# Performance work log

Measured on AMD Instinct MI355X. Metric: run time of the kernel, lower is better.

The kernel has to match this reference:

```python
import jax, jax.numpy as jnp
import numpy as np

N = 50000
E = 600000
D = 128
OUT = 40
NUM_ITERS = 5
GAMMA = 0.1
EPS = 0.1


def setup_inputs() -> dict:
    key = jax.random.key(0)
    ks = jax.random.split(key, 10)
    x = jax.random.normal(ks[0], (N, D), dtype=jnp.float32)
    edge_index = jax.random.randint(ks[1], (2, E), 0, N, dtype=jnp.int64)
    edge_weight = jax.random.uniform(ks[2], (E,), dtype=jnp.float32)
    s = 1.0 / np.sqrt(D)
    W_emb = jax.random.uniform(ks[3], (D, D), jnp.float32, -s, s)
    b_emb = jax.random.uniform(ks[4], (D,), jnp.float32, -s, s)
    W_lin = jax.random.uniform(ks[5], (D, D), jnp.float32, -s, s)
    W_anti = jax.random.uniform(ks[6], (D, D), jnp.float32, -s, s)
    b_conv = jax.random.uniform(ks[7], (D,), jnp.float32, -s, s)
    W_out = jax.random.uniform(ks[8], (OUT, D), jnp.float32, -s, s)
    b_out = jax.random.uniform(ks[9], (OUT,), jnp.float32, -s, s)
    return {"x": x, "edge_index": edge_index, "edge_weight": edge_weight,
            "W_emb": W_emb, "b_emb": b_emb, "W_lin": W_lin, "W_anti": W_anti,
            "b_conv": b_conv, "W_out": W_out, "b_out": b_out}


def reference(x, edge_index, edge_weight, W_emb, b_emb, W_lin, W_anti, b_conv, W_out, b_out):
    # input embedding: Linear(input_dim, hidden_dim)
    x = x @ W_emb.T + b_emb

    src = edge_index[0]  # x_j (messages gathered from source)
    dst = edge_index[1]  # aggregated at target via scatter-add

    # antisymmetric weight: W - W^T - gamma*I
    A = W_anti - W_anti.T - GAMMA * jnp.eye(D, dtype=x.dtype)

    def step(x, _):
        neigh = x @ W_lin.T                      # [N, D] linear transform
        msgs = neigh[src] * edge_weight[:, None]  # [E, D] gather + weight
        agg = jax.ops.segment_sum(msgs, dst, num_segments=N)  # scatter-add
        conv = x @ A.T + agg + b_conv
        x = x + EPS * jnp.tanh(conv)
        return x, None

    x, _ = jax.lax.scan(step, x, None, length=NUM_ITERS)

    # readout
    return x @ W_out.T + b_out
```

## Files before the change

kernel.cpp:

```cpp
#include <hip/hip_runtime.h>
#include <math.h>

#define N_NODES 50000
#define E_EDGES 600000
#define D_DIM 128
#define OUT_DIM 40
#define N_ITERS 5
#define GAMMA_C 0.1f
#define EPS_C 0.1f
#define SCAN_BLOCKS 196
#define GEMM_BLOCKS 391
#define CONV_BLOCKS 782
#define EDGE_BLOCKS_C 293

typedef short v8s __attribute__((ext_vector_type(8)));
typedef float v4f __attribute__((ext_vector_type(4)));
typedef unsigned int uint;
typedef unsigned short ushort;

__device__ __forceinline__ ushort f2bf(float f) {
    union { float f; uint u; } v; v.f = f;
    uint u = v.u;
    uint r = 0x7fffu + ((u >> 16) & 1u);
    return (ushort)((u + r) >> 16);
}
__device__ __forceinline__ float bf2f(ushort h) {
    union { uint u; float f; } v; v.u = ((uint)h) << 16;
    return v.f;
}
__device__ __forceinline__ float bflo(uint u) {
    union { uint u; float f; } v; v.u = u << 16; return v.f;
}
__device__ __forceinline__ float bfhi(uint u) {
    union { uint u; float f; } v; v.u = u & 0xffff0000u; return v.f;
}

__device__ __forceinline__ float tanh_fast(float x) {
    float e = __expf(x + x);
    return 1.0f - 2.0f * __builtin_amdgcn_rcpf(e + 1.0f);
}

__global__ __launch_bounds__(256) void zero_prep_kernel(int* __restrict__ cursor,
                                                        const float* __restrict__ Wemb,
                                                        const float* __restrict__ Wlin,
                                                        const float* __restrict__ Wanti,
                                                        const float* __restrict__ Wout,
                                                        ushort* __restrict__ WembH,
                                                        ushort* __restrict__ Wcat2H,
                                                        ushort* __restrict__ WoutH) {
    int i = blockIdx.x * 256 + threadIdx.x;
    if (i < N_NODES) cursor[i] = 0;
    if (i < D_DIM * D_DIM) {
        int r = i >> 7, c = i & 127;
        WembH[i] = f2bf(Wemb[i]);
        float a = Wanti[r * 128 + c] - Wanti[c * 128 + r];
        if (r == c) a -= GAMMA_C;
        Wcat2H[r * 256 + c]       = f2bf(a);
        Wcat2H[r * 256 + 128 + c] = f2bf(Wlin[r * 128 + c]);
        if (i < 48 * 128) WoutH[i] = (r < OUT_DIM) ? f2bf(Wout[r * 128 + c]) : (ushort)0;
    }
}

__global__ __launch_bounds__(256) void build_embed_kernel(
        const float* __restrict__ Xf, const ushort* __restrict__ Wh,
        const float* __restrict__ bias, ushort* __restrict__ xH,
        const int* __restrict__ src, const int* __restrict__ dst,
        const float* __restrict__ ew, int* __restrict__ cursor,
        int2* __restrict__ es2, int M) {
    __shared__ ushort Xs[128 * 128];
    const int tid = threadIdx.x;

    if (blockIdx.x >= GEMM_BLOCKS) {
        int base = (blockIdx.x - GEMM_BLOCKS) * 2048 + tid;
#pragma unroll
        for (int k = 0; k < 8; ++k) {
            int e = base + k * 256;
            if (e < E_EDGES) {
                int d = dst[e];
                int pos = atomicAdd(&cursor[d], 1);
                es2[pos] = make_int2(src[e], __float_as_int(ew[e]));
            }
        }
        return;
    }

    const int rowBase = blockIdx.x * 128;
#pragma unroll
    for (int p = 0; p < 8; ++p) {
        int cid = p * 256 + tid;
        int r = cid >> 4, c8 = cid & 15;
        int gr = rowBase + r;
        uint4 val = make_uint4(0, 0, 0, 0);
        if (gr < M) {
            const float* ptr = Xf + (size_t)gr * 128 + c8 * 8;
            float4 f0 = *(const float4*)ptr;
            float4 f1 = *(const float4*)(ptr + 4);
            val.x = (uint)f2bf(f0.x) | ((uint)f2bf(f0.y) << 16);
            val.y = (uint)f2bf(f0.z) | ((uint)f2bf(f0.w) << 16);
            val.z = (uint)f2bf(f1.x) | ((uint)f2bf(f1.y) << 16);
            val.w = (uint)f2bf(f1.z) | ((uint)f2bf(f1.w) << 16);
        }
        *(uint4*)(Xs + r * 128 + ((c8 ^ (r & 7)) << 3)) = val;
    }
    __syncthreads();

    const int lane = tid & 63;
    const int wv = tid >> 6;
    const int wrow = (wv & 1) * 64;
    const int wcol = (wv >> 1) * 64;
    const int l16 = lane & 15;
    const int q = lane >> 4;

    v4f acc[4][4];
#pragma unroll
    for (int i = 0; i < 4; ++i)
#pragma unroll
        for (int j = 0; j < 4; ++j) { v4f z = {0.f,0.f,0.f,0.f}; acc[i][j] = z; }

#pragma unroll
    for (int ks = 0; ks < 4; ++ks) {
        const int chunk = ks * 4 + q;
        v8s a[4], b[4];
#pragma unroll
        for (int i = 0; i < 4; ++i) {
            int m = wrow + i * 16 + l16;
            a[i] = *(const v8s*)(Xs + m * 128 + ((chunk ^ (m & 7)) << 3));
        }
#pragma unroll
        for (int j = 0; j < 4; ++j)
            b[j] = *(const v8s*)(Wh + (size_t)(wcol + j * 16 + l16) * 128 + chunk * 8);
#pragma unroll
        for (int i = 0; i < 4; ++i)
#pragma unroll
            for (int j = 0; j < 4; ++j)
                acc[i][j] = __builtin_amdgcn_mfma_f32_16x16x32_bf16(a[i], b[j], acc[i][j], 0, 0, 0);
    }

#pragma unroll
    for (int j = 0; j < 4; ++j) {
        int col = wcol + j * 16 + l16;
        float bj = bias[col];
#pragma unroll
        for (int i = 0; i < 4; ++i) {
            int grB = rowBase + wrow + i * 16 + q * 4;
#pragma unroll
            for (int r = 0; r < 4; ++r) {
                int gr = grB + r;
                if (gr < M) xH[(size_t)gr * 128 + col] = f2bf(acc[i][j][r] + bj);
            }
        }
    }
}

__global__ __launch_bounds__(512) void gather_conv_update(
        const ushort* __restrict__ xin, ushort* __restrict__ xout,
        const int2* __restrict__ es2, const int* __restrict__ rowStart,
        const int* __restrict__ rowEnd, const ushort* __restrict__ Wcat2,
        const float* __restrict__ bconv, const ushort* __restrict__ WoutH,
        const float* __restrict__ bout, float* __restrict__ out,
        int doOut, int M) {
    __shared__ ushort Xs0[64 * 128];
    __shared__ ushort Xs1[64 * 128];
    const int tid = threadIdx.x;
    const int rowBase = blockIdx.x * 64;

#pragma unroll
    for (int p = 0; p < 2; ++p) {
        int cid = p * 512 + tid;
        int r = cid >> 4, c8 = cid & 15;
        int gr = rowBase + r;
        uint4 xv = make_uint4(0, 0, 0, 0);
        if (gr < M) xv = *(const uint4*)(xin + (size_t)gr * 128 + c8 * 8);
        *(uint4*)(Xs1 + r * 128 + ((c8 ^ (r & 7)) << 3)) = xv;
    }

    const int q16 = tid & 15;
    const int nb = tid >> 4;
    const int gb = tid & 48;
    for (int pass = 0; pass < 2; ++pass) {
        int r = pass * 32 + nb;
        int gr = rowBase + r;
        float sA[8] = {0,0,0,0,0,0,0,0};
        float sB[8] = {0,0,0,0,0,0,0,0};
        int e0 = 0, deg = 0;
        if (gr < M) { e0 = rowStart[gr]; deg = rowEnd[gr] - e0; }
        for (int base = 0; base < deg; base += 16) {
            int idx = e0 + base + q16;
            int2 myE = es2[idx < E_EDGES ? idx : E_EDGES - 1];
            int cnt = deg - base; if (cnt > 16) cnt = 16;
            int k = 0;
            for (; k + 4 <= cnt; k += 4) {
                int s0 = __shfl(myE.x, gb + k + 0);
                int s1 = __shfl(myE.x, gb + k + 1);
                int s2 = __shfl(myE.x, gb + k + 2);
                int s3 = __shfl(myE.x, gb + k + 3);
                float w0 = __int_as_float(__shfl(myE.y, gb + k + 0));
                float w1 = __int_as_float(__shfl(myE.y, gb + k + 1));
                float w2 = __int_as_float(__shfl(myE.y, gb + k + 2));
                float w3 = __int_as_float(__shfl(myE.y, gb + k + 3));
                uint4 v0 = *(const uint4*)(xin + (size_t)s0 * 128 + q16 * 8);
                uint4 v1 = *(const uint4*)(xin + (size_t)s1 * 128 + q16 * 8);
                uint4 v2 = *(const uint4*)(xin + (size_t)s2 * 128 + q16 * 8);
                uint4 v3 = *(const uint4*)(xin + (size_t)s3 * 128 + q16 * 8);
                sA[0] = fmaf(w0, bflo(v0.x), sA[0]); sA[1] = fmaf(w0, bfhi(v0.x), sA[1]);
                sA[2] = fmaf(w0, bflo(v0.y), sA[2]); sA[3] = fmaf(w0, bfhi(v0.y), sA[3]);
                sA[4] = fmaf(w0, bflo(v0.z), sA[4]); sA[5] = fmaf(w0, bfhi(v0.z), sA[5]);
                sA[6] = fmaf(w0, bflo(v0.w), sA[6]); sA[7] = fmaf(w0, bfhi(v0.w), sA[7]);
                sB[0] = fmaf(w1, bflo(v1.x), sB[0]); sB[1] = fmaf(w1, bfhi(v1.x), sB[1]);
                sB[2] = fmaf(w1, bflo(v1.y), sB[2]); sB[3] = fmaf(w1, bfhi(v1.y), sB[3]);
                sB[4] = fmaf(w1, bflo(v1.z), sB[4]); sB[5] = fmaf(w1, bfhi(v1.z), sB[5]);
                sB[6] = fmaf(w1, bflo(v1.w), sB[6]); sB[7] = fmaf(w1, bfhi(v1.w), sB[7]);
                sA[0] = fmaf(w2, bflo(v2.x), sA[0]); sA[1] = fmaf(w2, bfhi(v2.x), sA[1]);
                sA[2] = fmaf(w2, bflo(v2.y), sA[2]); sA[3] = fmaf(w2, bfhi(v2.y), sA[3]);
                sA[4] = fmaf(w2, bflo(v2.z), sA[4]); sA[5] = fmaf(w2, bfhi(v2.z), sA[5]);
                sA[6] = fmaf(w2, bflo(v2.w), sA[6]); sA[7] = fmaf(w2, bfhi(v2.w), sA[7]);
                sB[0] = fmaf(w3, bflo(v3.x), sB[0]); sB[1] = fmaf(w3, bfhi(v3.x), sB[1]);
                sB[2] = fmaf(w3, bflo(v3.y), sB[2]); sB[3] = fmaf(w3, bfhi(v3.y), sB[3]);
                sB[4] = fmaf(w3, bflo(v3.z), sB[4]); sB[5] = fmaf(w3, bfhi(v3.z), sB[5]);
                sB[6] = fmaf(w3, bflo(v3.w), sB[6]); sB[7] = fmaf(w3, bfhi(v3.w), sB[7]);
            }
            for (; k < cnt; ++k) {
                int s = __shfl(myE.x, gb + k);
                float w = __int_as_float(__shfl(myE.y, gb + k));
                uint4 v = *(const uint4*)(xin + (size_t)s * 128 + q16 * 8);
                sA[0] = fmaf(w, bflo(v.x), sA[0]); sA[1] = fmaf(w, bfhi(v.x), sA[1]);
                sA[2] = fmaf(w, bflo(v.y), sA[2]); sA[3] = fmaf(w, bfhi(v.y), sA[3]);
                sA[4] = fmaf(w, bflo(v.z), sA[4]); sA[5] = fmaf(w, bfhi(v.z), sA[5]);
                sA[6] = fmaf(w, bflo(v.w), sA[6]); sA[7] = fmaf(w, bfhi(v.w), sA[7]);
            }
        }
        uint4 o;
        o.x = (uint)f2bf(sA[0] + sB[0]) | ((uint)f2bf(sA[1] + sB[1]) << 16);
        o.y = (uint)f2bf(sA[2] + sB[2]) | ((uint)f2bf(sA[3] + sB[3]) << 16);
        o.z = (uint)f2bf(sA[4] + sB[4]) | ((uint)f2bf(sA[5] + sB[5]) << 16);
        o.w = (uint)f2bf(sA[6] + sB[6]) | ((uint)f2bf(sA[7] + sB[7]) << 16);
        *(uint4*)(Xs0 + r * 128 + ((q16 ^ (r & 7)) << 3)) = o;
    }
    __syncthreads();

    const int lane = tid & 63;
    const int wv = tid >> 6;
    const int l16 = lane & 15;
    const int q = lane >> 4;

    v4f acc[4];
#pragma unroll
    for (int i = 0; i < 4; ++i) { v4f z = {0.f,0.f,0.f,0.f}; acc[i] = z; }

#pragma unroll
    for (int ks = 0; ks < 8; ++ks) {
        const ushort* Xsrc = (ks < 4) ? Xs0 : Xs1;
        const int wOff = (ks < 4) ? 128 : 0;
        const int chunk = (ks & 3) * 4 + q;
        v8s a[4], b;
#pragma unroll
        for (int i = 0; i < 4; ++i) {
            int m = i * 16 + l16;
            a[i] = *(const v8s*)(Xsrc + m * 128 + ((chunk ^ (m & 7)) << 3));
        }
        b = *(const v8s*)(Wcat2 + (size_t)(wv * 16 + l16) * 256 + wOff + chunk * 8);
#pragma unroll
        for (int i = 0; i < 4; ++i)
            acc[i] = __builtin_amdgcn_mfma_f32_16x16x32_bf16(a[i], b, acc[i], 0, 0, 0);
    }

    if (doOut) __syncthreads();

    {
        int col = wv * 16 + l16;
        float bj = bconv[col];
        const int csw = col >> 3, clo = col & 7;
#pragma unroll
        for (int i = 0; i < 4; ++i) {
            int trB = i * 16 + q * 4;
#pragma unroll
            for (int r = 0; r < 4; ++r) {
                int tr = trB + r;
                int gr = rowBase + tr;
                if (gr < M) {
                    int li = tr * 128 + (((csw ^ (tr & 7)) << 3) | clo);
                    float conv = acc[i][r] + bj;
                    float xv = bf2f(Xs1[li]) + EPS_C * tanh_fast(conv);
                    ushort h = f2bf(xv);
                    xout[(size_t)gr * 128 + col] = h;
                    if (doOut) Xs1[li] = h;
                }
            }
        }
    }

    if (doOut) {
        __syncthreads();
        if (wv < 4) {
            v4f acc2[3];
#pragma unroll
            for (int j = 0; j < 3; ++j) { v4f z = {0.f,0.f,0.f,0.f}; acc2[j] = z; }

#pragma unroll
            for (int ks = 0; ks < 4; ++ks) {
                const int chunk = ks * 4 + q;
                int m = wv * 16 + l16;
                v8s a2 = *(const v8s*)(Xs1 + m * 128 + ((chunk ^ (m & 7)) << 3));
                v8s b2[3];
#pragma unroll
                for (int j = 0; j < 3; ++j)
                    b2[j] = *(const v8s*)(WoutH + (size_t)(j * 16 + l16) * 128 + chunk * 8);
#pragma unroll
                for (int j = 0; j < 3; ++j)
                    acc2[j] = __builtin_amdgcn_mfma_f32_16x16x32_bf16(a2, b2[j], acc2[j], 0, 0, 0);
            }

#pragma unroll
            for (int j = 0; j < 3; ++j) {
                int col = j * 16 + l16;
                if (col >= OUT_DIM) continue;
                float bj = bout[col];
                int grB = rowBase + wv * 16 + q * 4;
#pragma unroll
                for (int r = 0; r < 4; ++r) {
                    int gr = grB + r;
                    if (gr < M) out[(size_t)gr * OUT_DIM + col] = acc2[j][r] + bj;
                }
            }
        }
    }
}

__global__ __launch_bounds__(256) void hist_kernel(const int* __restrict__ dst,
                                                   int* __restrict__ cnt) {
    int base = blockIdx.x * 2048 + threadIdx.x;
#pragma unroll
    for (int k = 0; k < 8; ++k) {
        int e = base + k * 256;
        if (e < E_EDGES) atomicAdd(&cnt[dst[e]], 1);
    }
}

__global__ __launch_bounds__(256) void scan_phase1(const int* __restrict__ deg,
                                                   int* __restrict__ localEx,
                                                   int* __restrict__ blockSums) {
    __shared__ int tmp[256];
    const int t = threadIdx.x;
    const int i = blockIdx.x * 256 + t;
    int v = (i < N_NODES) ? deg[i] : 0;
    tmp[t] = v;
    __syncthreads();
#pragma unroll
    for (int off = 1; off < 256; off <<= 1) {
        int u = (t >= off) ? tmp[t - off] : 0;
        __syncthreads();
        tmp[t] += u;
        __syncthreads();
    }
    if (i < N_NODES) localEx[i] = tmp[t] - v;
    if (t == 255) blockSums[blockIdx.x] = tmp[255];
}

__global__ __launch_bounds__(256) void scan_phase23(int* __restrict__ rowStart,
                                                    const int* __restrict__ blockSums,
                                                    int* __restrict__ cursor) {
    __shared__ int tmp[256];
    __shared__ int offs;
    const int t = threadIdx.x;
    int v = (t < SCAN_BLOCKS) ? blockSums[t] : 0;
    tmp[t] = v;
    __syncthreads();
#pragma unroll
    for (int off = 1; off < 256; off <<= 1) {
        int u = (t >= off) ? tmp[t - off] : 0;
        __syncthreads();
        tmp[t] += u;
        __syncthreads();
    }
    if (t == blockIdx.x) offs = tmp[t] - v;
    __syncthreads();
    const int i = blockIdx.x * 256 + t;
    if (i < N_NODES) {
        int val = rowStart[i] + offs;
        rowStart[i] = val;
        cursor[i] = val;
    }
}

extern "C" void kernel_launch(void* const* d_in, const int* in_sizes, int n_in,
                              void* d_out, int out_size, void* d_ws, size_t ws_size,
                              hipStream_t stream) {
    const float* x_in   = (const float*)d_in[0];
    const int*   ei     = (const int*)  d_in[1];
    const float* ew     = (const float*)d_in[2];
    const float* W_emb  = (const float*)d_in[3];
    const float* b_emb  = (const float*)d_in[4];
    const float* W_lin  = (const float*)d_in[5];
    const float* W_anti = (const float*)d_in[6];
    const float* b_conv = (const float*)d_in[7];
    const float* W_out  = (const float*)d_in[8];
    const float* b_out  = (const float*)d_in[9];
    float* out = (float*)d_out;

    ushort* xhA    = (ushort*)d_ws;
    ushort* xhB    = xhA + (size_t)N_NODES * D_DIM;
    ushort* WembH  = xhB + (size_t)N_NODES * D_DIM;
    ushort* Wcat2H = WembH + D_DIM * D_DIM;
    ushort* WoutH  = Wcat2H + 2 * D_DIM * D_DIM;
    int*    rowStart = (int*)(WoutH + 48 * D_DIM);
    int*    cursor   = rowStart + N_NODES;
    int2*   es2      = (int2*)(cursor + N_NODES);
    int*    blockSums = (int*)(es2 + E_EDGES);

    const int* src = ei;
    const int* dst = ei + E_EDGES;

    zero_prep_kernel<<<SCAN_BLOCKS, 256, 0, stream>>>(cursor, W_emb, W_lin, W_anti,
                                                      W_out, WembH, Wcat2H, WoutH);
    hist_kernel<<<EDGE_BLOCKS_C, 256, 0, stream>>>(dst, cursor);
    scan_phase1<<<SCAN_BLOCKS, 256, 0, stream>>>(cursor, rowStart, blockSums);
    scan_phase23<<<SCAN_BLOCKS, 256, 0, stream>>>(rowStart, blockSums, cursor);
    build_embed_kernel<<<GEMM_BLOCKS + EDGE_BLOCKS_C, 256, 0, stream>>>(
        x_in, WembH, b_emb, xhA, src, dst, ew, cursor, es2, N_NODES);

    ushort* bufs[2] = { xhA, xhB };
    for (int it = 0; it < N_ITERS; ++it) {
        gather_conv_update<<<CONV_BLOCKS, 512, 0, stream>>>(
            bufs[it & 1], bufs[(it + 1) & 1], es2, rowStart, cursor,
            Wcat2H, b_conv, WoutH, b_out, out,
            (it == N_ITERS - 1) ? 1 : 0, N_NODES);
    }
}
```

Baseline: 378.5 us.

## Halve rows per conv block, raise occupancy, unroll edge gather by eight

The fused gather/conv/update kernel now handles 32 rows per block instead of 64. That halves its shared memory and doubles the block count, and a min-blocks launch bound requests higher occupancy. The edge-gather loop gains an 8-wide unrolled path so more independent row loads are in flight, and the readout GEMM is redistributed over 6 waves. The aim is to hide the latency of the irregular gathers. In exchange, each block reuses the weight tile for fewer rows and may face register pressure under the occupancy bound.

```diff
diff --git a/kernel.cpp b/kernel.cpp
--- a/kernel.cpp
+++ b/kernel.cpp
@@ -10,7 +10,7 @@
 #define EPS_C 0.1f
 #define SCAN_BLOCKS 196
 #define GEMM_BLOCKS 391
-#define CONV_BLOCKS 782
+#define CONV_BLOCKS 1563
 #define EDGE_BLOCKS_C 293
 
 typedef short v8s __attribute__((ext_vector_type(8)));
@@ -152,22 +152,20 @@
     }
 }
 
-__global__ __launch_bounds__(512) void gather_conv_update(
+__global__ __launch_bounds__(512, 8) void gather_conv_update(
         const ushort* __restrict__ xin, ushort* __restrict__ xout,
         const int2* __restrict__ es2, const int* __restrict__ rowStart,
         const int* __restrict__ rowEnd, const ushort* __restrict__ Wcat2,
         const float* __restrict__ bconv, const ushort* __restrict__ WoutH,
         const float* __restrict__ bout, float* __restrict__ out,
         int doOut, int M) {
-    __shared__ ushort Xs0[64 * 128];
-    __shared__ ushort Xs1[64 * 128];
+    __shared__ ushort Xs0[32 * 128];
+    __shared__ ushort Xs1[32 * 128];
     const int tid = threadIdx.x;
-    const int rowBase = blockIdx.x * 64;
-
-#pragma unroll
-    for (int p = 0; p < 2; ++p) {
-        int cid = p * 512 + tid;
-        int r = cid >> 4, c8 = cid & 15;
+    const int rowBase = blockIdx.x * 32;
+
+    {
+        int r = tid >> 4, c8 = tid & 15;
         int gr = rowBase + r;
         uint4 xv = make_uint4(0, 0, 0, 0);
         if (gr < M) xv = *(const uint4*)(xin + (size_t)gr * 128 + c8 * 8);
@@ -177,8 +175,8 @@
     const int q16 = tid & 15;
     const int nb = tid >> 4;
     const int gb = tid & 48;
-    for (int pass = 0; pass < 2; ++pass) {
-        int r = pass * 32 + nb;
+    {
+        int r = nb;
         int gr = rowBase + r;
         float sA[8] = {0,0,0,0,0,0,0,0};
         float sB[8] = {0,0,0,0,0,0,0,0};
@@ -189,6 +187,64 @@
             int2 myE = es2[idx < E_EDGES ? idx : E_EDGES - 1];
             int cnt = deg - base; if (cnt > 16) cnt = 16;
             int k = 0;
+            for (; k + 8 <= cnt; k += 8) {
+                int s0 = __shfl(myE.x, gb + k + 0);
+                int s1 = __shfl(myE.x, gb + k + 1);
+                int s2 = __shfl(myE.x, gb + k + 2);
+                int s3 = __shfl(myE.x, gb + k + 3);
+                int s4 = __shfl(myE.x, gb + k + 4);
+                int s5 = __shfl(myE.x, gb + k + 5);
+                int s6 = __shfl(myE.x, gb + k + 6);
+                int s7 = __shfl(myE.x, gb + k + 7);
+                float w0 = __int_as_float(__shfl(myE.y, gb + k + 0));
+                float w1 = __int_as_float(__shfl(myE.y, gb + k + 1));
+                float w2 = __int_as_float(__shfl(myE.y, gb + k + 2));
+                float w3 = __int_as_float(__shfl(myE.y, gb + k + 3));
+                float w4 = __int_as_float(__shfl(myE.y, gb + k + 4));
+                float w5 = __int_as_float(__shfl(myE.y, gb + k + 5));
+                float w6 = __int_as_float(__shfl(myE.y, gb + k + 6));
+                float w7 = __int_as_float(__shfl(myE.y, gb + k + 7));
+                uint4 v0 = *(const uint4*)(xin + (size_t)s0 * 128 + q16 * 8);
+                uint4 v1 = *(const uint4*)(xin + (size_t)s1 * 128 + q16 * 8);
+                uint4 v2 = *(const uint4*)(xin + (size_t)s2 * 128 + q16 * 8);
+                uint4 v3 = *(const uint4*)(xin + (size_t)s3 * 128 + q16 * 8);
+                uint4 v4 = *(const uint4*)(xin + (size_t)s4 * 128 + q16 * 8);
+                uint4 v5 = *(const uint4*)(xin + (size_t)s5 * 128 + q16 * 8);
+                uint4 v6 = *(const uint4*)(xin + (size_t)s6 * 128 + q16 * 8);
+                uint4 v7 = *(const uint4*)(xin + (size_t)s7 * 128 + q16 * 8);
+                sA[0] = fmaf(w0, bflo(v0.x), sA[0]); sA[1] = fmaf(w0, bfhi(v0.x), sA[1]);
+                sA[2] = fmaf(w0, bflo(v0.y), sA[2]); sA[3] = fmaf(w0, bfhi(v0.y), sA[3]);
+                sA[4] = fmaf(w0, bflo(v0.z), sA[4]); sA[5] = fmaf(w0, bfhi(v0.z), sA[5]);
+                sA[6] = fmaf(w0, bflo(v0.w), sA[6]); sA[7] = fmaf(w0, bfhi(v0.w), sA[7]);
+                sB[0] = fmaf(w1, bflo(v1.x), sB[0]); sB[1] = fmaf(w1, bfhi(v1.x), sB[1]);
+                sB[2] = fmaf(w1, bflo(v1.y), sB[2]); sB[3] = fmaf(w1, bfhi(v1.y), sB[3]);
+                sB[4] = fmaf(w1, bflo(v1.z), sB[4]); sB[5] = fmaf(w1, bfhi(v1.z), sB[5]);
+                sB[6] = fmaf(w1, bflo(v1.w), sB[6]); sB[7] = fmaf(w1, bfhi(v1.w), sB[7]);
+                sA[0] = fmaf(w2, bflo(v2.x), sA[0]); sA[1] = fmaf(w2, bfhi(v2.x), sA[1]);
+                sA[2] = fmaf(w2, bflo(v2.y), sA[2]); sA[3] = fmaf(w2, bfhi(v2.y), sA[3]);
+                sA[4] = fmaf(w2, bflo(v2.z), sA[4]); sA[5] = fmaf(w2, bfhi(v2.z), sA[5]);
+                sA[6] = fmaf(w2, bflo(v2.w), sA[6]); sA[7] = fmaf(w2, bfhi(v2.w), sA[7]);
+                sB[0] = fmaf(w3, bflo(v3.x), sB[0]); sB[1] = fmaf(w3, bfhi(v3.x), sB[1]);
+                sB[2] = fmaf(w3, bflo(v3.y), sB[2]); sB[3] = fmaf(w3, bfhi(v3.y), sB[3]);
+                sB[4] = fmaf(w3, bflo(v3.z), sB[4]); sB[5] = fmaf(w3, bfhi(v3.z), sB[5]);
+                sB[6] = fmaf(w3, bflo(v3.w), sB[6]); sB[7] = fmaf(w3, bfhi(v3.w), sB[7]);
+                sA[0] = fmaf(w4, bflo(v4.x), sA[0]); sA[1] = fmaf(w4, bfhi(v4.x), sA[1]);
+                sA[2] = fmaf(w4, bflo(v4.y), sA[2]); sA[3] = fmaf(w4, bfhi(v4.y), sA[3]);
+                sA[4] = fmaf(w4, bflo(v4.z), sA[4]); sA[5] = fmaf(w4, bfhi(v4.z), sA[5]);
+                sA[6] = fmaf(w4, bflo(v4.w), sA[6]); sA[7] = fmaf(w4, bfhi(v4.w), sA[7]);
+                sB[0] = fmaf(w5, bflo(v5.x), sB[0]); sB[1] = fmaf(w5, bfhi(v5.x), sB[1]);
+                sB[2] = fmaf(w5, bflo(v5.y), sB[2]); sB[3] = fmaf(w5, bfhi(v5.y), sB[3]);
+                sB[4] = fmaf(w5, bflo(v5.z), sB[4]); sB[5] = fmaf(w5, bfhi(v5.z), sB[5]);
+                sB[6] = fmaf(w5, bflo(v5.w), sB[6]); sB[7] = fmaf(w5, bfhi(v5.w), sB[7]);
+                sA[0] = fmaf(w6, bflo(v6.x), sA[0]); sA[1] = fmaf(w6, bfhi(v6.x), sA[1]);
+                sA[2] = fmaf(w6, bflo(v6.y), sA[2]); sA[3] = fmaf(w6, bfhi(v6.y), sA[3]);
+                sA[4] = fmaf(w6, bflo(v6.z), sA[4]); sA[5] = fmaf(w6, bfhi(v6.z), sA[5]);
+                sA[6] = fmaf(w6, bflo(v6.w), sA[6]); sA[7] = fmaf(w6, bfhi(v6.w), sA[7]);
+                sB[0] = fmaf(w7, bflo(v7.x), sB[0]); sB[1] = fmaf(w7, bfhi(v7.x), sB[1]);
+                sB[2] = fmaf(w7, bflo(v7.y), sB[2]); sB[3] = fmaf(w7, bfhi(v7.y), sB[3]);
+                sB[4] = fmaf(w7, bflo(v7.z), sB[4]); sB[5] = fmaf(w7, bfhi(v7.z), sB[5]);
+                sB[6] = fmaf(w7, bflo(v7.w), sB[6]); sB[7] = fmaf(w7, bfhi(v7.w), sB[7]);
+            }
             for (; k + 4 <= cnt; k += 4) {
                 int s0 = __shfl(myE.x, gb + k + 0);
                 int s1 = __shfl(myE.x, gb + k + 1);
@@ -243,24 +299,24 @@
     const int l16 = lane & 15;
     const int q = lane >> 4;
 
-    v4f acc[4];
-#pragma unroll
-    for (int i = 0; i < 4; ++i) { v4f z = {0.f,0.f,0.f,0.f}; acc[i] = z; }
+    v4f acc[2];
+#pragma unroll
+    for (int i = 0; i < 2; ++i) { v4f z = {0.f,0.f,0.f,0.f}; acc[i] = z; }
 
 #pragma unroll
     for (int ks = 0; ks < 8; ++ks) {
         const ushort* Xsrc = (ks < 4) ? Xs0 : Xs1;
         const int wOff = (ks < 4) ? 128 : 0;
         const int chunk = (ks & 3) * 4 + q;
-        v8s a[4], b;
-#pragma unroll
-        for (int i = 0; i < 4; ++i) {
+        v8s a[2], b;
+#pragma unroll
+        for (int i = 0; i < 2; ++i) {
             int m = i * 16 + l16;
             a[i] = *(const v8s*)(Xsrc + m * 128 + ((chunk ^ (m & 7)) << 3));
         }
         b = *(const v8s*)(Wcat2 + (size_t)(wv * 16 + l16) * 256 + wOff + chunk * 8);
 #pragma unroll
-        for (int i = 0; i < 4; ++i)
+        for (int i = 0; i < 2; ++i)
             acc[i] = __builtin_amdgcn_mfma_f32_16x16x32_bf16(a[i], b, acc[i], 0, 0, 0);
     }
 
@@ -271,7 +327,7 @@
         float bj = bconv[col];
         const int csw = col >> 3, clo = col & 7;
 #pragma unroll
-        for (int i = 0; i < 4; ++i) {
+        for (int i = 0; i < 2; ++i) {
             int trB = i * 16 + q * 4;
 #pragma unroll
             for (int r = 0; r < 4; ++r) {
@@ -291,35 +347,25 @@
 
     if (doOut) {
         __syncthreads();
-        if (wv < 4) {
-            v4f acc2[3];
-#pragma unroll
-            for (int j = 0; j < 3; ++j) { v4f z = {0.f,0.f,0.f,0.f}; acc2[j] = z; }
-
+        if (wv < 6) {
+            const int rg = wv & 1, cg = wv >> 1;
+            v4f acc2 = {0.f, 0.f, 0.f, 0.f};
 #pragma unroll
             for (int ks = 0; ks < 4; ++ks) {
                 const int chunk = ks * 4 + q;
-                int m = wv * 16 + l16;
+                int m = rg * 16 + l16;
                 v8s a2 = *(const v8s*)(Xs1 + m * 128 + ((chunk ^ (m & 7)) << 3));
-                v8s b2[3];
-#pragma unroll
-                for (int j = 0; j < 3; ++j)
-                    b2[j] = *(const v8s*)(WoutH + (size_t)(j * 16 + l16) * 128 + chunk * 8);
-#pragma unroll
-                for (int j = 0; j < 3; ++j)
-                    acc2[j] = __builtin_amdgcn_mfma_f32_16x16x32_bf16(a2, b2[j], acc2[j], 0, 0, 0);
-            }
-
-#pragma unroll
-            for (int j = 0; j < 3; ++j) {
-                int col = j * 16 + l16;
-                if (col >= OUT_DIM) continue;
+                v8s b2 = *(const v8s*)(WoutH + (size_t)(cg * 16 + l16) * 128 + chunk * 8);
+                acc2 = __builtin_amdgcn_mfma_f32_16x16x32_bf16(a2, b2, acc2, 0, 0, 0);
+            }
+            int col = cg * 16 + l16;
+            if (col < OUT_DIM) {
                 float bj = bout[col];
-                int grB = rowBase + wv * 16 + q * 4;
+                int grB = rowBase + rg * 16 + q * 4;
 #pragma unroll
                 for (int r = 0; r < 4; ++r) {
                     int gr = grB + r;
-                    if (gr < M) out[(size_t)gr * OUT_DIM + col] = acc2[j][r] + bj;
+                    if (gr < M) out[(size_t)gr * OUT_DIM + col] = acc2[r] + bj;
                 }
             }
         }
```

Result: slower. 406.3 us (+7.3%).
